# Performance work log

Hardware: AMD Instinct MI355X
Metric: run time of the kernel (lower is better)

Reference implementation:

```python
import jax, jax.numpy as jnp
import numpy as np

N_NODES = 50000
N_EDGES = 800000
F_DIM = 64


def setup_inputs() -> dict:
    key = jax.random.key(0)
    ks = jax.random.split(key, 11)
    inp = {
        "x": jax.random.normal(ks[0], (1,), dtype=jnp.float32),  # unused by the module
        "features": jax.random.normal(ks[1], (N_NODES, F_DIM), dtype=jnp.float32),
        "edge_index": jax.random.randint(ks[2], (2, N_EDGES), 0, N_NODES, dtype=jnp.int64),
        # Conv2d(1, 8, (2,1)) -> weight (8,1,2,1) flattened to (8,2)
        "conv_w": jax.random.normal(ks[3], (8, 2), dtype=jnp.float32) * (1.0 / np.sqrt(2.0)),
        "conv_b": jax.random.normal(ks[4], (8,), dtype=jnp.float32) * 0.1,
        "w1": jax.random.normal(ks[5], (16, F_DIM), dtype=jnp.float32) * (1.0 / np.sqrt(F_DIM)),
        "b1": jax.random.normal(ks[6], (16,), dtype=jnp.float32) * 0.1,
        "w2": jax.random.normal(ks[7], (1, 16), dtype=jnp.float32) * (1.0 / np.sqrt(16.0)),
        "b2": jax.random.normal(ks[8], (1,), dtype=jnp.float32) * 0.1,
        "w3": jax.random.normal(ks[9], (1, 8), dtype=jnp.float32) * (1.0 / np.sqrt(8.0)),
        "b3": jax.random.normal(ks[10], (1,), dtype=jnp.float32) * 0.1,
    }
    return inp


def reference(x, features, edge_index, conv_w, conv_b, w1, b1, w2, b2, w3, b3):
    # Gather endpoint features for each edge: (E, F) each
    src, dst = edge_index[0], edge_index[1]
    f1 = features[src]
    f2 = features[dst]
    # Conv2d(1,8,(2,1)) on (E,1,2,F) collapses the 2-row stack:
    # out[e,o,f] = w[o,0]*f1[e,f] + w[o,1]*f2[e,f] + b[o]
    feat = (f1[:, None, :] * conv_w[None, :, 0, None]
            + f2[:, None, :] * conv_w[None, :, 1, None]
            + conv_b[None, :, None])          # (E, 8, F)
    feat = jax.nn.relu(feat)
    # fc1: Linear(F, 16) applied over last dim -> (E, 8, 16)
    feat = jax.nn.relu(jnp.einsum('eof,gf->eog', feat, w1) + b1)
    # fc2: Linear(16, 1) -> (E, 8, 1) -> reshape (E, 8)
    feat = jax.nn.relu(jnp.einsum('eog,hg->eoh', feat, w2) + b2)
    feat = feat.reshape(-1, 8)
    # fc3: Linear(8, 1) + sigmoid -> (E, 1)
    out = jax.nn.sigmoid(feat @ w3.T + b3)
    return out
```

## Files before the change

kernel.cpp:

```cpp
#include <hip/hip_runtime.h>
#include <hip/hip_bf16.h>


typedef _Float16 f16x8 __attribute__((ext_vector_type(8)));
typedef _Float16 f16x4 __attribute__((ext_vector_type(4)));
typedef _Float16 f16x2 __attribute__((ext_vector_type(2)));
typedef short    bf16x8 __attribute__((ext_vector_type(8)));
typedef float    f32x4  __attribute__((ext_vector_type(4)));
typedef float    f32x2  __attribute__((ext_vector_type(2)));

union U8 { f16x8 v; f16x2 p[4]; };

static __device__ __forceinline__ short f2bf(float f) {
    union { __hip_bfloat16 h; short s; } u;
    u.h = __float2bfloat16(f);
    return u.s;
}

__global__ __launch_bounds__(256) void feat_to_f16(const float* __restrict__ in,
                                                   _Float16* __restrict__ out,
                                                   int n4) {
    int i = blockIdx.x * blockDim.x + threadIdx.x;
    const int stride = gridDim.x * blockDim.x;
    for (; i < n4; i += stride) {
        const f32x4 v = ((const f32x4*)in)[i];
        ((f16x4*)out)[i] = __builtin_convertvector(v, f16x4);
    }
}

__global__ __launch_bounds__(256, 8) void edgeconv_f16_glds(
    const _Float16* __restrict__ feat16,
    const int*      __restrict__ edge_index,
    const float* __restrict__ conv_w, const float* __restrict__ conv_b,
    const float* __restrict__ w1,     const float* __restrict__ b1,
    const float* __restrict__ w2,     const float* __restrict__ b2,
    const float* __restrict__ w3,     const float* __restrict__ b3,
    float* __restrict__ out, int nEdges)
{
    __shared__ __align__(16) char smem[4][4][1024];

    const int tid = threadIdx.x;
    const int l   = tid & 63;
    const int wid = tid >> 6;
    const int grp = l >> 4;
    const int n   = l & 15;
    const int ch  = l & 7;
    const int el  = (l >> 3) & 1;
    const int chunk = l & 7;
    const int rr    = l >> 3;
    const int eloc  = rr >> 1;
    const int endp  = rr & 1;

    const float* w1r = w1 + n * 64 + grp * 8;
    f16x8 aw0, aw1;
    #pragma unroll
    for (int i = 0; i < 8; ++i) {
        aw0[i] = (_Float16)w1r[i];
        aw1[i] = (_Float16)w1r[32 + i];
    }

    const _Float16 cah = (_Float16)conv_w[2 * ch];
    const _Float16 cch = (_Float16)conv_w[2 * ch + 1];
    const _Float16 cbh = (_Float16)conv_b[ch];
    const f16x2 vca = {cah, cah}, vcc = {cch, cch}, vcb = {cbh, cbh};
    const f16x2 vzero = {(_Float16)0.f, (_Float16)0.f};

    f32x4 accInit;
    float w2r[4];
    #pragma unroll
    for (int r = 0; r < 4; ++r) {
        accInit[r] = b1[grp * 4 + r];
        w2r[r]     = w2[grp * 4 + r];
    }
    const float w3v = w3[ch];
    const float b2v = b2[0];
    const float b3v = b3[0];

    const int nGroups    = (nEdges + 15) >> 4;
    const int totalWaves = gridDim.x * 4;
    int g = blockIdx.x * 4 + wid;
    if (g >= nGroups) return;

    int ce = min(g * 16 + n, nEdges - 1);
    int vs = edge_index[ce];
    int vd = edge_index[nEdges + ce];

    char* myLds = (char*)&smem[wid][0][0];

    while (true) {
        #pragma unroll
        for (int p = 0; p < 4; ++p) {
            const int si  = __shfl(vs, 4 * p + eloc);
            const int di  = __shfl(vd, 4 * p + eloc);
            const int idx = endp ? di : si;
            const char* ga = (const char*)feat16
                           + (size_t)(unsigned)idx * 128u + chunk * 16;
            __builtin_amdgcn_global_load_lds(
                (const __attribute__((address_space(1))) void*)ga,
                (__attribute__((address_space(3))) void*)(myLds + p * 1024),
                16, 0, 0);
        }

        const int gn    = g + totalWaves;
        const bool more = (gn < nGroups);
        int vsn = 0, vdn = 0;
        if (more) {
            const int cen = min(gn * 16 + n, nEdges - 1);
            vsn = edge_index[cen];
            vdn = edge_index[nEdges + cen];
        }

        float zp[8];
        #pragma unroll
        for (int p = 0; p < 4; ++p) {
            if      (p == 0) asm volatile("s_waitcnt vmcnt(3)" ::: "memory");
            else if (p == 1) asm volatile("s_waitcnt vmcnt(2)" ::: "memory");
            else if (p == 2) asm volatile("s_waitcnt vmcnt(1)" ::: "memory");
            else             asm volatile("s_waitcnt vmcnt(0)" ::: "memory");
            __builtin_amdgcn_sched_barrier(0);

            const char* pb = myLds + p * 1024;
            #pragma unroll
            for (int q = 0; q < 2; ++q) {
                const int roff = q * 512 + el * 256 + grp * 16;
                U8 s0_, s1_, d0_, d1_, c0, c1;
                s0_.v = *(const f16x8*)(pb + roff);
                s1_.v = *(const f16x8*)(pb + roff + 64);
                d0_.v = *(const f16x8*)(pb + roff + 128);
                d1_.v = *(const f16x8*)(pb + roff + 192);

                #pragma unroll
                for (int pp = 0; pp < 4; ++pp) {
                    f16x2 tL = __builtin_elementwise_fma(vca, s0_.p[pp],
                                __builtin_elementwise_fma(vcc, d0_.p[pp], vcb));
                    c0.p[pp] = __builtin_elementwise_max(tL, vzero);
                    f16x2 tH = __builtin_elementwise_fma(vca, s1_.p[pp],
                                __builtin_elementwise_fma(vcc, d1_.p[pp], vcb));
                    c1.p[pp] = __builtin_elementwise_max(tH, vzero);
                }

                f32x4 acc = accInit;
                acc = __builtin_amdgcn_mfma_f32_16x16x32_f16(aw0, c0.v, acc, 0, 0, 0);
                acc = __builtin_amdgcn_mfma_f32_16x16x32_f16(aw1, c1.v, acc, 0, 0, 0);

                float z_ = 0.f;
                #pragma unroll
                for (int r = 0; r < 4; ++r) {
                    const float h1 = fmaxf(acc[r], 0.f);
                    z_ = fmaf(h1, w2r[r], z_);
                }
                zp[2 * p + q] = z_;
            }
        }

        #pragma unroll
        for (int t = 0; t < 8; ++t) zp[t] += __shfl_xor(zp[t], 16);
        #pragma unroll
        for (int t = 0; t < 8; ++t) zp[t] += __shfl_xor(zp[t], 32);
        #pragma unroll
        for (int t = 0; t < 8; ++t) {
            const float h2 = fmaxf(zp[t] + b2v, 0.f);
            zp[t] = h2 * w3v;
        }
        #pragma unroll
        for (int t = 0; t < 8; ++t) zp[t] += __shfl_xor(zp[t], 1);
        #pragma unroll
        for (int t = 0; t < 8; ++t) zp[t] += __shfl_xor(zp[t], 2);
        #pragma unroll
        for (int t = 0; t < 8; ++t) zp[t] += __shfl_xor(zp[t], 4);
        #pragma unroll
        for (int t = 0; t < 8; ++t) {
            const float z  = zp[t] + b3v;
            const float sg = 1.0f / (1.0f + __expf(-z));
            if ((l & 55) == 0) {
                const int e = g * 16 + 2 * t + (l >> 3);
                if (e < nEdges) out[e] = sg;
            }
        }

        if (!more) break;
        g = gn; vs = vsn; vd = vdn;
    }
}

__global__ __launch_bounds__(256) void edgeconv_mfma2(
    const float* __restrict__ features, const int* __restrict__ edge_index,
    const float* __restrict__ conv_w, const float* __restrict__ conv_b,
    const float* __restrict__ w1, const float* __restrict__ b1,
    const float* __restrict__ w2, const float* __restrict__ b2,
    const float* __restrict__ w3, const float* __restrict__ b3,
    float* __restrict__ out, int nEdges)
{
    const int tid = threadIdx.x;
    const int l   = tid & 63;
    const int wid = tid >> 6;
    const int grp = l >> 4;
    const int n   = l & 15;
    const int ch  = l & 7;
    const int el  = (l >> 3) & 1;

    const float* w1r = w1 + n * 64 + grp * 8;
    bf16x8 aw0, aw1;
    #pragma unroll
    for (int i = 0; i < 8; ++i) {
        aw0[i] = f2bf(w1r[i]);
        aw1[i] = f2bf(w1r[32 + i]);
    }
    const float ca = conv_w[2 * ch];
    const float cc = conv_w[2 * ch + 1];
    const float cb = conv_b[ch];
    float b1r[4], w2r[4];
    #pragma unroll
    for (int r = 0; r < 4; ++r) { b1r[r] = b1[grp * 4 + r]; w2r[r] = w2[grp * 4 + r]; }
    const float w3v = w3[ch];
    const float b2v = b2[0];
    const float b3v = b3[0];

    const int ebase = (blockIdx.x * 4 + wid) * 16;
    const int ce    = min(ebase + n, nEdges - 1);
    const int vs    = edge_index[ce];
    const int vd    = edge_index[nEdges + ce];

#define LOAD_TILE4(T, X1, X2) do { \
    const int sn_ = __shfl(vs, 2 * (T) + el); \
    const int dn_ = __shfl(vd, 2 * (T) + el); \
    const float* p1_ = features + (size_t)sn_ * 64 + grp * 8; \
    const float* p2_ = features + (size_t)dn_ * 64 + grp * 8; \
    X1[0] = *(const f32x4*)(p1_);      X1[1] = *(const f32x4*)(p1_ + 4); \
    X1[2] = *(const f32x4*)(p1_ + 32); X1[3] = *(const f32x4*)(p1_ + 36); \
    X2[0] = *(const f32x4*)(p2_);      X2[1] = *(const f32x4*)(p2_ + 4); \
    X2[2] = *(const f32x4*)(p2_ + 32); X2[3] = *(const f32x4*)(p2_ + 36); \
} while (0)

    f32x4 x1v[4], x2v[4];
    LOAD_TILE4(0, x1v, x2v);
    const f32x2 vca = {ca, ca}, vcc = {cc, cc}, vcb = {cb, cb};
    const f32x2 vz  = {0.f, 0.f};

    #pragma unroll
    for (int t = 0; t < 8; ++t) {
        f32x4 n1v[4], n2v[4];
        if (t < 7) LOAD_TILE4(t + 1, n1v, n2v);
        bf16x8 cf0, cf1;
        #pragma unroll
        for (int p = 0; p < 8; ++p) {
            const int q = p >> 1;
            const int o = (p & 1) * 2;
            f32x2 u = {x1v[q][o], x1v[q][o + 1]};
            f32x2 v = {x2v[q][o], x2v[q][o + 1]};
            f32x2 tt = __builtin_elementwise_fma(vca, u,
                        __builtin_elementwise_fma(vcc, v, vcb));
            tt = __builtin_elementwise_max(tt, vz);
            const short s0 = f2bf(tt[0]), s1 = f2bf(tt[1]);
            if (p < 4) { cf0[2 * (p & 3)] = s0; cf0[2 * (p & 3) + 1] = s1; }
            else       { cf1[2 * (p & 3)] = s0; cf1[2 * (p & 3) + 1] = s1; }
        }
        f32x4 acc = {0.f, 0.f, 0.f, 0.f};
        acc = __builtin_amdgcn_mfma_f32_16x16x32_bf16(aw0, cf0, acc, 0, 0, 0);
        acc = __builtin_amdgcn_mfma_f32_16x16x32_bf16(aw1, cf1, acc, 0, 0, 0);
        float zp = 0.f;
        #pragma unroll
        for (int r = 0; r < 4; ++r) {
            const float h1 = fmaxf(acc[r] + b1r[r], 0.f);
            zp = fmaf(h1, w2r[r], zp);
        }
        zp += __shfl_xor(zp, 16);
        zp += __shfl_xor(zp, 32);
        const float h2 = fmaxf(zp + b2v, 0.f);
        float t3 = h2 * w3v;
        t3 += __shfl_xor(t3, 1);
        t3 += __shfl_xor(t3, 2);
        t3 += __shfl_xor(t3, 4);
        const float z  = t3 + b3v;
        const float sg = 1.0f / (1.0f + __expf(-z));
        if ((l & 55) == 0) {
            const int e = ebase + 2 * t + (l >> 3);
            if (e < nEdges) out[e] = sg;
        }
        if (t < 7) {
            #pragma unroll
            for (int i = 0; i < 4; ++i) { x1v[i] = n1v[i]; x2v[i] = n2v[i]; }
        }
    }
#undef LOAD_TILE4
}

extern "C" void kernel_launch(void* const* d_in, const int* in_sizes, int n_in,
                              void* d_out, int out_size, void* d_ws, size_t ws_size,
                              hipStream_t stream) {
    const float* features = (const float*)d_in[1];
    const int*   edge_idx = (const int*)d_in[2];
    const float* conv_w   = (const float*)d_in[3];
    const float* conv_b   = (const float*)d_in[4];
    const float* w1       = (const float*)d_in[5];
    const float* b1       = (const float*)d_in[6];
    const float* w2       = (const float*)d_in[7];
    const float* b2       = (const float*)d_in[8];
    const float* w3       = (const float*)d_in[9];
    const float* b3       = (const float*)d_in[10];
    float*       out      = (float*)d_out;

    const int nEdges = in_sizes[2] / 2;
    const int nFeat  = in_sizes[1];

    const size_t need = (size_t)nFeat * sizeof(_Float16);
    if (ws_size >= need) {
        _Float16* feat16 = (_Float16*)d_ws;
        feat_to_f16<<<2048, 256, 0, stream>>>(features, feat16, nFeat / 4);
        const int nGroups = (nEdges + 15) >> 4;
        const int blocks  = min(2048, (nGroups + 3) / 4);
        edgeconv_f16_glds<<<blocks, 256, 0, stream>>>(feat16, edge_idx,
                                                      conv_w, conv_b, w1, b1, w2, b2, w3, b3,
                                                      out, nEdges);
    } else {
        const dim3 grid((nEdges + 63) / 64);
        edgeconv_mfma2<<<grid, 256, 0, stream>>>(features, edge_idx,
                                                 conv_w, conv_b, w1, b1, w2, b2, w3, b3,
                                                 out, nEdges);
    }
}
```

Before: 81.02 us.

## Double-buffer LDS gather so next edge group loads during compute

The gather kernel now keeps two LDS buffers per wave and issues the global-to-LDS feature loads for the next edge group before computing the current one, so gather latency overlaps with MFMA work. Edge indices are prefetched two groups ahead. LDS per block doubles to 32 KB, launch bounds drop to 4 blocks per SM and the grid is capped at 1024 blocks. This trades fewer resident waves and less latency hiding through occupancy for explicit software pipelining.

```diff
diff --git a/kernel.cpp b/kernel.cpp
--- a/kernel.cpp
+++ b/kernel.cpp
@@ -28,7 +28,7 @@
     }
 }
 
-__global__ __launch_bounds__(256, 8) void edgeconv_f16_glds(
+__global__ __launch_bounds__(256, 4) void edgeconv_f16_dbuf(
     const _Float16* __restrict__ feat16,
     const int*      __restrict__ edge_index,
     const float* __restrict__ conv_w, const float* __restrict__ conv_b,
@@ -37,7 +37,7 @@
     const float* __restrict__ w3,     const float* __restrict__ b3,
     float* __restrict__ out, int nEdges)
 {
-    __shared__ __align__(16) char smem[4][4][1024];
+    __shared__ __align__(16) char smem[4][2][4][1024];
 
     const int tid = threadIdx.x;
     const int l   = tid & 63;
@@ -81,76 +81,93 @@
     int g = blockIdx.x * 4 + wid;
     if (g >= nGroups) return;
 
+    char* base0 = (char*)&smem[wid][0][0][0];
+    char* base1 = (char*)&smem[wid][1][0][0];
+
+#define ISSUE(VS, VD, BUF) do { \
+    _Pragma("unroll") \
+    for (int p_ = 0; p_ < 4; ++p_) { \
+        const int si_  = __shfl((VS), 4 * p_ + eloc); \
+        const int di_  = __shfl((VD), 4 * p_ + eloc); \
+        const int idx_ = endp ? di_ : si_; \
+        const char* ga_ = (const char*)feat16 \
+                        + (size_t)(unsigned)idx_ * 128u + chunk * 16; \
+        __builtin_amdgcn_global_load_lds( \
+            (const __attribute__((address_space(1))) void*)ga_, \
+            (__attribute__((address_space(3))) void*)((BUF) + p_ * 1024), \
+            16, 0, 0); \
+    } \
+} while (0)
+
     int ce = min(g * 16 + n, nEdges - 1);
     int vs = edge_index[ce];
     int vd = edge_index[nEdges + ce];
-
-    char* myLds = (char*)&smem[wid][0][0];
-
+    ISSUE(vs, vd, base0);
+
+    int gn = g + totalWaves;
+    int vs1 = 0, vd1 = 0;
+    if (gn < nGroups) {
+        const int cen = min(gn * 16 + n, nEdges - 1);
+        vs1 = edge_index[cen];
+        vd1 = edge_index[nEdges + cen];
+    }
+
+    int cur = 0;
     while (true) {
-        #pragma unroll
-        for (int p = 0; p < 4; ++p) {
-            const int si  = __shfl(vs, 4 * p + eloc);
-            const int di  = __shfl(vd, 4 * p + eloc);
-            const int idx = endp ? di : si;
-            const char* ga = (const char*)feat16
-                           + (size_t)(unsigned)idx * 128u + chunk * 16;
-            __builtin_amdgcn_global_load_lds(
-                (const __attribute__((address_space(1))) void*)ga,
-                (__attribute__((address_space(3))) void*)(myLds + p * 1024),
-                16, 0, 0);
-        }
-
-        const int gn    = g + totalWaves;
         const bool more = (gn < nGroups);
-        int vsn = 0, vdn = 0;
+
         if (more) {
-            const int cen = min(gn * 16 + n, nEdges - 1);
-            vsn = edge_index[cen];
-            vdn = edge_index[nEdges + cen];
-        }
-
+            ISSUE(vs1, vd1, (cur ? base0 : base1));
+            __builtin_amdgcn_sched_barrier(0);
+            asm volatile("s_waitcnt vmcnt(4)" ::: "memory");
+        } else {
+            asm volatile("s_waitcnt vmcnt(0)" ::: "memory");
+        }
+        __builtin_amdgcn_sched_barrier(0);
+
+        const int g2 = gn + totalWaves;
+        int vs2 = 0, vd2 = 0;
+        if (g2 < nGroups) {
+            const int ce2 = min(g2 * 16 + n, nEdges - 1);
+            vs2 = edge_index[ce2];
+            vd2 = edge_index[nEdges + ce2];
+        }
+
+        const char* myBuf = cur ? base1 : base0;
         float zp[8];
         #pragma unroll
-        for (int p = 0; p < 4; ++p) {
-            if      (p == 0) asm volatile("s_waitcnt vmcnt(3)" ::: "memory");
-            else if (p == 1) asm volatile("s_waitcnt vmcnt(2)" ::: "memory");
-            else if (p == 2) asm volatile("s_waitcnt vmcnt(1)" ::: "memory");
-            else             asm volatile("s_waitcnt vmcnt(0)" ::: "memory");
-            __builtin_amdgcn_sched_barrier(0);
-
-            const char* pb = myLds + p * 1024;
+        for (int t = 0; t < 8; ++t) {
+            const int p = t >> 1;
+            const int q = t & 1;
+            const char* pb = myBuf + p * 1024;
+            const int roff = q * 512 + el * 256 + grp * 16;
+            U8 s0_, s1_, d0_, d1_, c0, c1;
+            s0_.v = *(const f16x8*)(pb + roff);
+            s1_.v = *(const f16x8*)(pb + roff + 64);
+            d0_.v = *(const f16x8*)(pb + roff + 128);
+            d1_.v = *(const f16x8*)(pb + roff + 192);
+
             #pragma unroll
-            for (int q = 0; q < 2; ++q) {
-                const int roff = q * 512 + el * 256 + grp * 16;
-                U8 s0_, s1_, d0_, d1_, c0, c1;
-                s0_.v = *(const f16x8*)(pb + roff);
-                s1_.v = *(const f16x8*)(pb + roff + 64);
-                d0_.v = *(const f16x8*)(pb + roff + 128);
-                d1_.v = *(const f16x8*)(pb + roff + 192);
-
-                #pragma unroll
-                for (int pp = 0; pp < 4; ++pp) {
-                    f16x2 tL = __builtin_elementwise_fma(vca, s0_.p[pp],
-                                __builtin_elementwise_fma(vcc, d0_.p[pp], vcb));
-                    c0.p[pp] = __builtin_elementwise_max(tL, vzero);
-                    f16x2 tH = __builtin_elementwise_fma(vca, s1_.p[pp],
-                                __builtin_elementwise_fma(vcc, d1_.p[pp], vcb));
-                    c1.p[pp] = __builtin_elementwise_max(tH, vzero);
-                }
-
-                f32x4 acc = accInit;
-                acc = __builtin_amdgcn_mfma_f32_16x16x32_f16(aw0, c0.v, acc, 0, 0, 0);
-                acc = __builtin_amdgcn_mfma_f32_16x16x32_f16(aw1, c1.v, acc, 0, 0, 0);
-
-                float z_ = 0.f;
-                #pragma unroll
-                for (int r = 0; r < 4; ++r) {
-                    const float h1 = fmaxf(acc[r], 0.f);
-                    z_ = fmaf(h1, w2r[r], z_);
-                }
-                zp[2 * p + q] = z_;
+            for (int pp = 0; pp < 4; ++pp) {
+                f16x2 tL = __builtin_elementwise_fma(vca, s0_.p[pp],
+                            __builtin_elementwise_fma(vcc, d0_.p[pp], vcb));
+                c0.p[pp] = __builtin_elementwise_max(tL, vzero);
+                f16x2 tH = __builtin_elementwise_fma(vca, s1_.p[pp],
+                            __builtin_elementwise_fma(vcc, d1_.p[pp], vcb));
+                c1.p[pp] = __builtin_elementwise_max(tH, vzero);
             }
+
+            f32x4 acc = accInit;
+            acc = __builtin_amdgcn_mfma_f32_16x16x32_f16(aw0, c0.v, acc, 0, 0, 0);
+            acc = __builtin_amdgcn_mfma_f32_16x16x32_f16(aw1, c1.v, acc, 0, 0, 0);
+
+            float z_ = 0.f;
+            #pragma unroll
+            for (int r = 0; r < 4; ++r) {
+                const float h1 = fmaxf(acc[r], 0.f);
+                z_ = fmaf(h1, w2r[r], z_);
+            }
+            zp[t] = z_;
         }
 
         #pragma unroll
@@ -179,8 +196,9 @@
         }
 
         if (!more) break;
-        g = gn; vs = vsn; vd = vdn;
-    }
+        g = gn; gn = g2; vs1 = vs2; vd1 = vd2; cur ^= 1;
+    }
+#undef ISSUE
 }
 
 __global__ __launch_bounds__(256) void edgeconv_mfma2(
@@ -308,8 +326,8 @@
         _Float16* feat16 = (_Float16*)d_ws;
         feat_to_f16<<<2048, 256, 0, stream>>>(features, feat16, nFeat / 4);
         const int nGroups = (nEdges + 15) >> 4;
-        const int blocks  = min(2048, (nGroups + 3) / 4);
-        edgeconv_f16_glds<<<blocks, 256, 0, stream>>>(feat16, edge_idx,
+        const int blocks  = min(1024, (nGroups + 3) / 4);
+        edgeconv_f16_dbuf<<<blocks, 256, 0, stream>>>(feat16, edge_idx,
                                                       conv_w, conv_b, w1, b1, w2, b2, w3, b3,
                                                       out, nEdges);
     } else {
```

New measurement: 78.68 us. 1.03x faster.
